# Performance work log

Hardware: AMD Instinct MI355X
Metric: run time of the kernel (lower is better)

## Reference

```python
import jax, jax.numpy as jnp
import numpy as np

B, D_IN, H = 16384, 512, 1024


def setup_inputs() -> dict:
    key = jax.random.key(0)
    ks = jax.random.split(key, 12)
    s_in = 1.0 / np.sqrt(D_IN)
    s_h = 1.0 / np.sqrt(H)
    d = {
        "input_x": jax.random.normal(ks[0], (B, D_IN), jnp.float32),
        "h_old": jax.random.normal(ks[1], (B, H), jnp.float32),
        "c_old": jax.random.normal(ks[2], (B, H), jnp.float32),
    }
    names_U = ["Ui", "Uf", "Uo", "Uc"]
    names_W = ["Wi", "Wf", "Wo", "Wc"]
    for i, n in enumerate(names_U):
        d[n + "_w"] = jax.random.normal(ks[3 + i], (D_IN, H), jnp.float32) * s_in
        d[n + "_b"] = jnp.zeros((H,), jnp.float32)
    for i, n in enumerate(names_W):
        d[n + "_w"] = jax.random.normal(ks[7 + i], (H, H), jnp.float32) * s_h
        d[n + "_b"] = jnp.zeros((H,), jnp.float32)
    return d


def reference(input_x, h_old, c_old,
              Ui_w, Ui_b, Wi_w, Wi_b,
              Uf_w, Uf_b, Wf_w, Wf_b,
              Uo_w, Uo_b, Wo_w, Wo_b,
              Uc_w, Uc_b, Wc_w, Wc_b):
    # Fuse the 8 small GEMMs into 2: concatenate gate projections along the
    # output dim (math identical to 8 separate Dense layers + adds).
    U = jnp.concatenate([Ui_w, Uf_w, Uo_w, Uc_w], axis=1)   # [D_in, 4H]
    W = jnp.concatenate([Wi_w, Wf_w, Wo_w, Wc_w], axis=1)   # [H, 4H]
    b = jnp.concatenate([Ui_b + Wi_b, Uf_b + Wf_b, Uo_b + Wo_b, Uc_b + Wc_b])
    gates = input_x @ U + h_old @ W + b                      # [B, 4H]
    i_t, f_t, o_t, g_t = jnp.split(gates, 4, axis=1)
    i_t = jax.nn.sigmoid(i_t)
    f_t = jax.nn.sigmoid(f_t)
    o_t = jax.nn.sigmoid(o_t)
    c_t = jnp.tanh(g_t)
    c = i_t * c_t + f_t * c_old
    h_new = o_t * jnp.tanh(c)
    return (h_new, c)
```

## Files before the change

kernel.cpp:

```cpp
#include <hip/hip_runtime.h>
#include <hip/hip_bf16.h>
#include <stdint.h>

#define B_ROWS 16384
#define D_IN   512
#define H_DIM  1024
#define K_TOT  1536
#define NKT    48

typedef __attribute__((ext_vector_type(8)))  short bf16x8;
typedef __attribute__((ext_vector_type(4)))  float f32x4;
typedef __attribute__((ext_vector_type(4)))  float float4v;
typedef __attribute__((ext_vector_type(8)))  unsigned short u16x8;

__device__ __forceinline__ unsigned short f2bf(float f) {
    uint32_t u = __float_as_uint(f);
    u = (u + 0x7FFFu + ((u >> 16) & 1u)) >> 16;
    return (unsigned short)u;
}

__global__ void cvt_A(const float* __restrict__ x, const float* __restrict__ h,
                      unsigned short* __restrict__ Ag) {
    int t     = blockIdx.x * blockDim.x + threadIdx.x;
    int lane  = t & 63;
    int chunk = (t >> 6) & 7;
    int rest  = t >> 9;
    int tile  = rest % 48;
    int bm    = rest / 48;
    int row   = bm * 128 + chunk * 16 + (lane & 15);
    int k     = tile * 32 + (lane >> 4) * 8;
    const float* src = (k < 512) ? (x + (size_t)row * D_IN + k)
                                 : (h + (size_t)row * H_DIM + (k - 512));
    float4v v0 = *(const float4v*)(src);
    float4v v1 = *(const float4v*)(src + 4);
    u16x8 o;
    o[0] = f2bf(v0[0]); o[1] = f2bf(v0[1]); o[2] = f2bf(v0[2]); o[3] = f2bf(v0[3]);
    o[4] = f2bf(v1[0]); o[5] = f2bf(v1[1]); o[6] = f2bf(v1[2]); o[7] = f2bf(v1[3]);
    *(u16x8*)(Ag + (size_t)t * 8) = o;
}

__global__ void cvt_B(const float* __restrict__ Ui, const float* __restrict__ Uf,
                      const float* __restrict__ Uo, const float* __restrict__ Uc,
                      const float* __restrict__ Wi, const float* __restrict__ Wf,
                      const float* __restrict__ Wo, const float* __restrict__ Wc,
                      unsigned short* __restrict__ Bg) {
    int t     = blockIdx.x * blockDim.x + threadIdx.x;
    int lane  = t & 63;
    int chunk = (t >> 6) & 7;
    int rest  = t >> 9;
    int tile  = rest % 48;
    int bn    = rest / 48;
    int c     = bn * 128 + chunk * 16 + (lane & 15);
    int g     = (c >> 4) & 3;
    int hcol  = ((c >> 6) << 4) | (c & 15);
    int k     = tile * 32 + (lane >> 4) * 8;
    const float* up = (g == 0) ? Ui : (g == 1) ? Uf : (g == 2) ? Uo : Uc;
    const float* wp = (g == 0) ? Wi : (g == 1) ? Wf : (g == 2) ? Wo : Wc;
    u16x8 o;
    if (k < 512) {
        const float* s = up + (size_t)k * H_DIM + hcol;
        #pragma unroll
        for (int i = 0; i < 8; ++i) o[i] = f2bf(s[(size_t)i * H_DIM]);
    } else {
        const float* s = wp + (size_t)(k - 512) * H_DIM + hcol;
        #pragma unroll
        for (int i = 0; i < 8; ++i) o[i] = f2bf(s[(size_t)i * H_DIM]);
    }
    *(u16x8*)(Bg + (size_t)t * 8) = o;
}

__global__ void cvt_bias(const float* __restrict__ Uib, const float* __restrict__ Ufb,
                         const float* __restrict__ Uob, const float* __restrict__ Ucb,
                         const float* __restrict__ Wib, const float* __restrict__ Wfb,
                         const float* __restrict__ Wob, const float* __restrict__ Wcb,
                         float* __restrict__ bias) {
    int t = blockIdx.x * blockDim.x + threadIdx.x;
    int g = t >> 10, h = t & 1023;
    const float* ub = (g == 0) ? Uib : (g == 1) ? Ufb : (g == 2) ? Uob : Ucb;
    const float* wb = (g == 0) ? Wib : (g == 1) ? Wfb : (g == 2) ? Wob : Wcb;
    bias[t] = ub[h] + wb[h];
}

__global__ __launch_bounds__(256, 4) void lstm_gemm(
        const unsigned short* __restrict__ Ag, const unsigned short* __restrict__ Bg,
        const float* __restrict__ bias, const float* __restrict__ c_old,
        float* __restrict__ out) {
    __shared__ __align__(1024) char lds[49152];

    const int tid = threadIdx.x;
    const int l   = tid & 63;
    const int wv  = tid >> 6;
    const int wm  = wv >> 1;
    const int wn  = wv & 1;

    const int orig = blockIdx.x;
    const int xcd  = orig & 7;
    const int j    = orig >> 3;
    const int bn   = xcd * 4 + (j & 3);
    const int bm   = j >> 2;

    const unsigned short* aCur = Ag + ((size_t)bm * 48 * 8 + 2 * wv) * 512 + l * 8;
    const unsigned short* bCur = Bg + ((size_t)bn * 48 * 8 + 2 * wv) * 512 + l * 8;

    const int aRd = wm * 4096 + l * 16;
    const int bRd = 8192 + wn * 4096 + l * 16;

#define GLDS(SRC, DST) __builtin_amdgcn_global_load_lds(                            \
        (const __attribute__((address_space(1))) void*)(SRC),                       \
        (__attribute__((address_space(3))) void*)(DST), 16, 0, 0)

#define STAGE(SLOTBASE) do {                                                        \
    char* _da = (char*)lds + (SLOTBASE) + wv * 2048;                                \
    GLDS(aCur, _da);            GLDS(aCur + 512, _da + 1024);                       \
    GLDS(bCur, _da + 8192);     GLDS(bCur + 512, _da + 8192 + 1024);                \
    aCur += 4096; bCur += 4096;                                                     \
} while (0)

    f32x4 acc[4][4] = {};

#define PHASE(SLOT) do {                                                            \
    const char* _b = (const char*)lds + (SLOT) * 16384;                             \
    bf16x8 aF[4], bF[4];                                                            \
    _Pragma("unroll") for (int m = 0; m < 4; ++m)                                   \
        aF[m] = *(const bf16x8*)(_b + aRd + m * 1024);                              \
    _Pragma("unroll") for (int n = 0; n < 4; ++n)                                   \
        bF[n] = *(const bf16x8*)(_b + bRd + n * 1024);                              \
    STAGE(((((SLOT) + 2) % 3)) * 16384);                                            \
    __builtin_amdgcn_s_setprio(1);                                                  \
    _Pragma("unroll") for (int m = 0; m < 4; ++m)                                   \
        _Pragma("unroll") for (int n = 0; n < 4; ++n)                               \
            acc[m][n] = __builtin_amdgcn_mfma_f32_16x16x32_bf16(                    \
                aF[m], bF[n], acc[m][n], 0, 0, 0);                                  \
    __builtin_amdgcn_s_setprio(0);                                                  \
    asm volatile("s_waitcnt vmcnt(4)\ns_barrier" ::: "memory");                     \
} while (0)

    STAGE(0); STAGE(16384);
    asm volatile("s_waitcnt vmcnt(4)\ns_barrier" ::: "memory");

    #pragma unroll 1
    for (int i = 0; i < 15; ++i) {
        PHASE(0);
        PHASE(1);
        PHASE(2);
    }
    PHASE(0);
    aCur -= (size_t)48 * 4096;  bCur -= (size_t)48 * 4096;
    PHASE(1);
    PHASE(2);
    asm volatile("s_waitcnt vmcnt(0)" ::: "memory");

    const int hh  = bn * 32 + wn * 16 + (l & 15);
    const float bi  = bias[hh];
    const float bff = bias[1024 + hh];
    const float bo  = bias[2048 + hh];
    const float bc  = bias[3072 + hh];

    #pragma unroll
    for (int m = 0; m < 4; ++m) {
        const int rb = bm * 128 + wm * 64 + m * 16 + ((l >> 4) * 4);
        #pragma unroll
        for (int jj = 0; jj < 4; ++jj) {
            const int r = rb + jj;
            float iv = acc[m][0][jj] + bi;
            float fv = acc[m][1][jj] + bff;
            float ov = acc[m][2][jj] + bo;
            float gv = acc[m][3][jj] + bc;
            float it = 1.f / (1.f + __expf(-iv));
            float ft = 1.f / (1.f + __expf(-fv));
            float ot = 1.f / (1.f + __expf(-ov));
            float gt = 1.f - 2.f / (1.f + __expf(2.f * gv));
            float co = c_old[(size_t)r * H_DIM + hh];
            float cn = it * gt + ft * co;
            float th = 1.f - 2.f / (1.f + __expf(2.f * cn));
            out[(size_t)r * H_DIM + hh] = ot * th;
            out[(size_t)B_ROWS * H_DIM + (size_t)r * H_DIM + hh] = cn;
        }
    }
#undef PHASE
#undef STAGE
#undef GLDS
}

extern "C" void kernel_launch(void* const* d_in, const int* in_sizes, int n_in,
                              void* d_out, int out_size, void* d_ws, size_t ws_size,
                              hipStream_t stream) {
    const float* x  = (const float*)d_in[0];
    const float* h0 = (const float*)d_in[1];
    const float* c0 = (const float*)d_in[2];
    const float* Uw[4] = {(const float*)d_in[3],  (const float*)d_in[5],
                          (const float*)d_in[7],  (const float*)d_in[9]};
    const float* Ub[4] = {(const float*)d_in[4],  (const float*)d_in[6],
                          (const float*)d_in[8],  (const float*)d_in[10]};
    const float* Ww[4] = {(const float*)d_in[11], (const float*)d_in[13],
                          (const float*)d_in[15], (const float*)d_in[17]};
    const float* Wb[4] = {(const float*)d_in[12], (const float*)d_in[14],
                          (const float*)d_in[16], (const float*)d_in[18]};

    unsigned short* Ag = (unsigned short*)d_ws;
    unsigned short* Bg = Ag + (size_t)B_ROWS * K_TOT;
    float* bias        = (float*)(Bg + (size_t)4096 * K_TOT);
    float* out         = (float*)d_out;

    cvt_A<<<12288, 256, 0, stream>>>(x, h0, Ag);
    cvt_B<<<3072, 256, 0, stream>>>(Uw[0], Uw[1], Uw[2], Uw[3],
                                    Ww[0], Ww[1], Ww[2], Ww[3], Bg);
    cvt_bias<<<16, 256, 0, stream>>>(Ub[0], Ub[1], Ub[2], Ub[3],
                                     Wb[0], Wb[1], Wb[2], Wb[3], bias);
    lstm_gemm<<<4096, 256, 0, stream>>>(Ag, Bg, bias, c0, out);
}
```

Measured before the change: 285.2 us.

## Enlarge GEMM tiles to 256x256 with 8 waves and double-buffered 64-K stages

The fused LSTM GEMM moves from 128x128 tiles with 4 waves and a 3-slot 32-K ring to 256x256 tiles with 8 waves, 128 KB of LDS and two 64-K buffers split into half-K phases. B fragments are kept in registers across two A sub-phases. The repack kernels change their layouts to match. The aim is higher arithmetic intensity per LDS and global byte. In exchange there are more barriers per tile, only one block per CU, and 1024 blocks, which may leave some CUs idle at the tail.

```diff
diff --git a/kernel.cpp b/kernel.cpp
--- a/kernel.cpp
+++ b/kernel.cpp
@@ -6,7 +6,7 @@
 #define D_IN   512
 #define H_DIM  1024
 #define K_TOT  1536
-#define NKT    48
+#define NT64   24
 
 typedef __attribute__((ext_vector_type(8)))  short bf16x8;
 typedef __attribute__((ext_vector_type(4)))  float f32x4;
@@ -23,12 +23,13 @@
                       unsigned short* __restrict__ Ag) {
     int t     = blockIdx.x * blockDim.x + threadIdx.x;
     int lane  = t & 63;
-    int chunk = (t >> 6) & 7;
-    int rest  = t >> 9;
-    int tile  = rest % 48;
-    int bm    = rest / 48;
-    int row   = bm * 128 + chunk * 16 + (lane & 15);
-    int k     = tile * 32 + (lane >> 4) * 8;
+    int chunk = (t >> 6) & 15;
+    int kh    = (t >> 10) & 1;
+    int rest  = t >> 11;
+    int T     = rest % 24;
+    int bm    = rest / 24;
+    int row   = bm * 256 + chunk * 16 + (lane & 15);
+    int k     = T * 64 + kh * 32 + (lane >> 4) * 8;
     const float* src = (k < 512) ? (x + (size_t)row * D_IN + k)
                                  : (h + (size_t)row * H_DIM + (k - 512));
     float4v v0 = *(const float4v*)(src);
@@ -46,14 +47,15 @@
                       unsigned short* __restrict__ Bg) {
     int t     = blockIdx.x * blockDim.x + threadIdx.x;
     int lane  = t & 63;
-    int chunk = (t >> 6) & 7;
-    int rest  = t >> 9;
-    int tile  = rest % 48;
-    int bn    = rest / 48;
-    int c     = bn * 128 + chunk * 16 + (lane & 15);
+    int chunk = (t >> 6) & 15;
+    int kh    = (t >> 10) & 1;
+    int rest  = t >> 11;
+    int T     = rest % 24;
+    int bn    = rest / 24;
+    int c     = bn * 256 + chunk * 16 + (lane & 15);
     int g     = (c >> 4) & 3;
     int hcol  = ((c >> 6) << 4) | (c & 15);
-    int k     = tile * 32 + (lane >> 4) * 8;
+    int k     = T * 64 + kh * 32 + (lane >> 4) * 8;
     const float* up = (g == 0) ? Ui : (g == 1) ? Uf : (g == 2) ? Uo : Uc;
     const float* wp = (g == 0) ? Wi : (g == 1) ? Wf : (g == 2) ? Wo : Wc;
     u16x8 o;
@@ -81,91 +83,104 @@
     bias[t] = ub[h] + wb[h];
 }
 
-__global__ __launch_bounds__(256, 4) void lstm_gemm(
+__global__ __launch_bounds__(512) void lstm_gemm(
         const unsigned short* __restrict__ Ag, const unsigned short* __restrict__ Bg,
         const float* __restrict__ bias, const float* __restrict__ c_old,
         float* __restrict__ out) {
-    __shared__ __align__(1024) char lds[49152];
+    __shared__ __align__(1024) char lds[131072];
 
     const int tid = threadIdx.x;
     const int l   = tid & 63;
     const int wv  = tid >> 6;
-    const int wm  = wv >> 1;
-    const int wn  = wv & 1;
+    const int wm  = wv >> 2;
+    const int wn  = wv & 3;
 
     const int orig = blockIdx.x;
     const int xcd  = orig & 7;
-    const int j    = orig >> 3;
-    const int bn   = xcd * 4 + (j & 3);
-    const int bm   = j >> 2;
-
-    const unsigned short* aCur = Ag + ((size_t)bm * 48 * 8 + 2 * wv) * 512 + l * 8;
-    const unsigned short* bCur = Bg + ((size_t)bn * 48 * 8 + 2 * wv) * 512 + l * 8;
-
-    const int aRd = wm * 4096 + l * 16;
-    const int bRd = 8192 + wn * 4096 + l * 16;
+    const int jj   = orig >> 3;
+    const int bn   = (xcd & 3) * 4 + (jj & 3);
+    const int bm   = (xcd >> 2) * 32 + (jj >> 2);
+
+    const unsigned short* aSrc = Ag + (size_t)bm * 24 * 16384 + tid * 8;
+    const unsigned short* bSrc = Bg + (size_t)bn * 24 * 16384 + tid * 8;
+
+    const int aRd = wm * 8192 + l * 16;
+    const int bRd = wn * 4096 + l * 16;
 
 #define GLDS(SRC, DST) __builtin_amdgcn_global_load_lds(                            \
         (const __attribute__((address_space(1))) void*)(SRC),                       \
         (__attribute__((address_space(3))) void*)(DST), 16, 0, 0)
 
-#define STAGE(SLOTBASE) do {                                                        \
-    char* _da = (char*)lds + (SLOTBASE) + wv * 2048;                                \
-    GLDS(aCur, _da);            GLDS(aCur + 512, _da + 1024);                       \
-    GLDS(bCur, _da + 8192);     GLDS(bCur + 512, _da + 8192 + 1024);                \
-    aCur += 4096; bCur += 4096;                                                     \
+#define STAGE(MAT, T, KH, BUF) do {                                                 \
+    const unsigned short* _s = ((MAT) ? bSrc : aSrc) + (size_t)((T) * 2 + (KH)) * 8192; \
+    char* _d = (char*)lds + (BUF) * 65536 + (MAT) * 32768 + (KH) * 16384 + wv * 1024;   \
+    GLDS(_s, _d);  GLDS(_s + 4096, _d + 8192);                                      \
 } while (0)
 
-    f32x4 acc[4][4] = {};
-
-#define PHASE(SLOT) do {                                                            \
-    const char* _b = (const char*)lds + (SLOT) * 16384;                             \
-    bf16x8 aF[4], bF[4];                                                            \
+    f32x4 acc[8][4] = {};
+    bf16x8 bPers[4];
+
+#define PHASE(BUF, KH, Q, RB, SM, ST, SKH, SBUF, GATE) do {                         \
+    const char* _Ab = (const char*)lds + (BUF) * 65536 + (KH) * 16384 + aRd;        \
+    bf16x8 aF[4];                                                                   \
     _Pragma("unroll") for (int m = 0; m < 4; ++m)                                   \
-        aF[m] = *(const bf16x8*)(_b + aRd + m * 1024);                              \
-    _Pragma("unroll") for (int n = 0; n < 4; ++n)                                   \
-        bF[n] = *(const bf16x8*)(_b + bRd + n * 1024);                              \
-    STAGE(((((SLOT) + 2) % 3)) * 16384);                                            \
+        aF[m] = *(const bf16x8*)(_Ab + ((Q) * 4 + m) * 1024);                       \
+    if (RB) {                                                                       \
+        const char* _Bb = (const char*)lds + (BUF) * 65536 + 32768 + (KH) * 16384 + bRd; \
+        _Pragma("unroll") for (int n = 0; n < 4; ++n)                               \
+            bPers[n] = *(const bf16x8*)(_Bb + n * 1024);                            \
+    }                                                                               \
+    STAGE(SM, ST, SKH, SBUF);                                                       \
+    __builtin_amdgcn_s_barrier();                                                   \
+    asm volatile("s_waitcnt lgkmcnt(0)" ::: "memory");                              \
+    __builtin_amdgcn_sched_barrier(0);                                              \
     __builtin_amdgcn_s_setprio(1);                                                  \
     _Pragma("unroll") for (int m = 0; m < 4; ++m)                                   \
         _Pragma("unroll") for (int n = 0; n < 4; ++n)                               \
-            acc[m][n] = __builtin_amdgcn_mfma_f32_16x16x32_bf16(                    \
-                aF[m], bF[n], acc[m][n], 0, 0, 0);                                  \
+            acc[(Q) * 4 + m][n] = __builtin_amdgcn_mfma_f32_16x16x32_bf16(          \
+                aF[m], bPers[n], acc[(Q) * 4 + m][n], 0, 0, 0);                     \
     __builtin_amdgcn_s_setprio(0);                                                  \
-    asm volatile("s_waitcnt vmcnt(4)\ns_barrier" ::: "memory");                     \
+    if (GATE) { asm volatile("s_waitcnt vmcnt(4)\ns_barrier" ::: "memory"); }       \
+    else      { asm volatile("s_barrier" ::: "memory"); }                           \
 } while (0)
 
-    STAGE(0); STAGE(16384);
+    STAGE(0, 0, 0, 0); STAGE(1, 0, 0, 0);
+    STAGE(0, 0, 1, 0); STAGE(1, 0, 1, 0);
+    STAGE(0, 1, 0, 1); STAGE(1, 1, 0, 1);
     asm volatile("s_waitcnt vmcnt(4)\ns_barrier" ::: "memory");
 
     #pragma unroll 1
-    for (int i = 0; i < 15; ++i) {
-        PHASE(0);
-        PHASE(1);
-        PHASE(2);
+    for (int i = 0; i < 12; ++i) {
+        const int t1 = 2 * i + 1;
+        int t2 = 2 * i + 2; if (t2 >= NT64) t2 -= NT64;
+        int t3 = 2 * i + 3; if (t3 >= NT64) t3 -= NT64;
+        PHASE(0, 0, 0, 1,  0, t1, 1, 1,  0);
+        PHASE(0, 0, 1, 0,  1, t1, 1, 1,  0);
+        PHASE(0, 1, 0, 1,  0, t2, 0, 0,  0);
+        PHASE(0, 1, 1, 0,  1, t2, 0, 0,  1);
+        PHASE(1, 0, 0, 1,  0, t2, 1, 0,  0);
+        PHASE(1, 0, 1, 0,  1, t2, 1, 0,  0);
+        PHASE(1, 1, 0, 1,  0, t3, 0, 1,  0);
+        PHASE(1, 1, 1, 0,  1, t3, 0, 1,  1);
     }
-    PHASE(0);
-    aCur -= (size_t)48 * 4096;  bCur -= (size_t)48 * 4096;
-    PHASE(1);
-    PHASE(2);
     asm volatile("s_waitcnt vmcnt(0)" ::: "memory");
 
-    const int hh  = bn * 32 + wn * 16 + (l & 15);
+    const int hh  = (bn * 4 + wn) * 16 + (l & 15);
     const float bi  = bias[hh];
     const float bff = bias[1024 + hh];
     const float bo  = bias[2048 + hh];
     const float bc  = bias[3072 + hh];
 
     #pragma unroll
-    for (int m = 0; m < 4; ++m) {
-        const int rb = bm * 128 + wm * 64 + m * 16 + ((l >> 4) * 4);
+    for (int a = 0; a < 8; ++a) {
+        const int rb = bm * 256 + wm * 128 + (a >> 2) * 64 + (a & 3) * 16 + ((l >> 4) * 4);
         #pragma unroll
-        for (int jj = 0; jj < 4; ++jj) {
-            const int r = rb + jj;
-            float iv = acc[m][0][jj] + bi;
-            float fv = acc[m][1][jj] + bff;
-            float ov = acc[m][2][jj] + bo;
-            float gv = acc[m][3][jj] + bc;
+        for (int j = 0; j < 4; ++j) {
+            const int r = rb + j;
+            float iv = acc[a][0][j] + bi;
+            float fv = acc[a][1][j] + bff;
+            float ov = acc[a][2][j] + bo;
+            float gv = acc[a][3][j] + bc;
             float it = 1.f / (1.f + __expf(-iv));
             float ft = 1.f / (1.f + __expf(-fv));
             float ot = 1.f / (1.f + __expf(-ov));
@@ -207,5 +222,5 @@
                                     Ww[0], Ww[1], Ww[2], Ww[3], Bg);
     cvt_bias<<<16, 256, 0, stream>>>(Ub[0], Ub[1], Ub[2], Ub[3],
                                      Wb[0], Wb[1], Wb[2], Wb[3], bias);
-    lstm_gemm<<<4096, 256, 0, stream>>>(Ag, Bg, bias, c0, out);
-}
+    lstm_gemm<<<1024, 512, 0, stream>>>(Ag, Bg, bias, c0, out);
+}
```

Result: faster. 256.7 us (median of 2 runs) (-10.0%).
